# Optimization experiments

Measured on AMD Instinct MI355X. Metric: run time of the kernel, lower is better.

The kernel has to match this reference:

```python
import jax, jax.numpy as jnp
import numpy as np

THRESHOLD = 1.0  # LIF firing threshold (single-step LIF: spike = heaviside(v - thr))


def _lif_spike(v):
    # single-step LIF: membrane = input, spike where membrane exceeds threshold
    return (v > THRESHOLD).astype(v.dtype)


def setup_inputs() -> dict:
    key = jax.random.key(0)
    ks = jax.random.split(key, 9)
    B, T, C = 2, 2048, 1024
    s = 1.0 / np.sqrt(C)
    return {
        "x": jax.random.normal(ks[0], (B, T, C), dtype=jnp.float32),
        "Wq": jax.random.normal(ks[1], (C, C), dtype=jnp.float32) * s,
        "bq": jnp.zeros((C,), dtype=jnp.float32),
        "Wk": jax.random.normal(ks[2], (C, C), dtype=jnp.float32) * s,
        "bk": jnp.zeros((C,), dtype=jnp.float32),
        "Wv": jax.random.normal(ks[3], (C, C), dtype=jnp.float32) * s,
        "bv": jnp.zeros((C,), dtype=jnp.float32),
        "Wo": jax.random.normal(ks[4], (C, C), dtype=jnp.float32) * s,
        "bo": jnp.zeros((C,), dtype=jnp.float32),
    }


def reference(x, Wq, bq, Wk, bk, Wv, bv, Wo, bo):
    B, T, C = x.shape
    H = 16
    D = C // H
    q = x @ Wq.T + bq
    k = x @ Wk.T + bk
    v = x @ Wv.T + bv
    # LIF spiking on q and k (binary spikes)
    qs = _lif_spike(q).reshape(B, T, H, D).transpose(0, 2, 1, 3)  # [B,H,T,D]
    ks = _lif_spike(k).reshape(B, T, H, D).transpose(0, 2, 1, 3)  # [B,H,T,D]
    vh = v.reshape(B, T, H, D).transpose(0, 2, 1, 3)              # [B,H,T,D]
    scores = jnp.einsum('bhqd,bhkd->bhqk', qs, ks) / jnp.sqrt(jnp.asarray(D, x.dtype))
    attn = jax.nn.softmax(scores, axis=-1)
    out = jnp.einsum('bhqk,bhkd->bhqd', attn, vh)                 # [B,H,T,D]
    out = out.transpose(0, 2, 1, 3).reshape(B, T, C)
    return out @ Wo.T + bo
```

## Files before the change

kernel.cpp:

```cpp
#include <hip/hip_runtime.h>
#include <cstdint>

typedef unsigned long long u64;
typedef unsigned int u32;
typedef unsigned short u16;
typedef __attribute__((ext_vector_type(8))) u16 u16x8;
typedef __attribute__((ext_vector_type(4))) u16 u16x4;
typedef __attribute__((ext_vector_type(8))) _Float16 f16x8;
typedef __attribute__((ext_vector_type(4))) float f32x4;

#define T_LEN 2048
#define C_DIM 1024
#define H_NUM 16
#define M_ROWS 4096
#define MB (1024ull * 1024ull)
#define TAU 3e-3f
#define FCAP 65536u
#define BLK_FCAP 512u

__device__ __forceinline__ u16 f2bf(float f) {
  unsigned u = __builtin_bit_cast(unsigned, f);
  return (u16)((u + 0x7FFFu + ((u >> 16) & 1u)) >> 16);
}
__device__ __forceinline__ u16 f2h(float f) {
  _Float16 h = (_Float16)f;
  return __builtin_bit_cast(u16, h);
}

__device__ __forceinline__ void async16(u16* lds, const u16* g) {
  __builtin_amdgcn_global_load_lds(
      (const __attribute__((address_space(1))) void*)g,
      (__attribute__((address_space(3))) void*)lds, 16, 0, 0);
}

__global__ __launch_bounds__(256) void split_all(
    const float* __restrict__ x,  const float* __restrict__ Wq,
    const float* __restrict__ Wk, const float* __restrict__ Wv,
    const float* __restrict__ Wo,
    u16* xh, u16* wq16, u16* wk16, u16* wv16, u16* woh, u32* flagcnt)
{
  const int i = blockIdx.x * 256 + threadIdx.x;
  if (i == 0) *flagcnt = 0;
  const float* src; u16* dst; int off; int isbf = 0;
  if      (i < 1048576) { src = x;  dst = xh;   off = i; }
  else if (i < 1310720) { src = Wq; dst = wq16; off = i - 1048576; }
  else if (i < 1572864) { src = Wk; dst = wk16; off = i - 1310720; }
  else if (i < 1835008) { src = Wv; dst = wv16; off = i - 1572864; }
  else                  { src = Wo; dst = woh;  off = i - 1835008; isbf = 1; }
  const float4 v = ((const float4*)src)[off];
  u16x4 h;
  if (isbf) {
    h[0] = f2bf(v.x); h[1] = f2bf(v.y); h[2] = f2bf(v.z); h[3] = f2bf(v.w);
  } else {
    h[0] = f2h(v.x);  h[1] = f2h(v.y);  h[2] = f2h(v.z);  h[3] = f2h(v.w);
  }
  ((u16x4*)dst)[off] = h;
}

__global__ __launch_bounds__(256) void mfma_qkv(
    const u16* __restrict__ A16,
    const u16* __restrict__ Bq16, const u16* __restrict__ Bk16,
    const u16* __restrict__ Bv16,
    const float* __restrict__ bq, const float* __restrict__ bk,
    const float* __restrict__ bv,
    u32* __restrict__ pbits, u32* __restrict__ flagcnt,
    u32* __restrict__ flaglist, u16* __restrict__ vT)
{
  __shared__ u16 Ahs[2][128][32];
  __shared__ u16 Bhs[2][64][32];
  __shared__ u32 fls[2 + BLK_FCAP];

  const int tid  = threadIdx.x;
  const int lane = tid & 63;
  const int w    = tid >> 6;
  const int wr   = w & 1;
  const int wc   = w >> 1;
  const int bm   = blockIdx.x * 128;
  const int bng  = blockIdx.y * 64;
  const int sel  = bng >> 10;
  const int bnl  = bng & 1023;

  const u16* Bh = (sel == 0) ? Bq16 : (sel == 1) ? Bk16 : Bv16;
  const float* bias = (sel == 0) ? bq : (sel == 1) ? bk : bv;

  if (tid == 0) fls[0] = 0;

  f32x4 acc[4][2];
  #pragma unroll
  for (int mf = 0; mf < 4; ++mf)
    #pragma unroll
    for (int nf = 0; nf < 2; ++nf) acc[mf][nf] = (f32x4){0.f, 0.f, 0.f, 0.f};

  const int sr = lane >> 2;
  const int sc = lane & 3;

#define STG(DST, SRC, TB, R0, KT)                                          \
  async16(&DST[(R0)][0],                                                   \
          &SRC[(size_t)((TB) + (R0) + sr) * 1024 + (KT) +                  \
               ((sc ^ ((((R0) + sr) >> 1) & 3)) << 3)]);

#define STAGE(B_, KT)                        \
  {                                          \
    STG(Ahs[B_], A16, bm, w * 32, KT);       \
    STG(Ahs[B_], A16, bm, w * 32 + 16, KT);  \
    STG(Bhs[B_], Bh, bnl, w * 16, KT);       \
  }

  STAGE(0, 0);
  __syncthreads();

  const int fr = lane & 15;
  const int fg = lane >> 4;
  int cur = 0;

  for (int kt = 0; kt < 1024; kt += 32) {
    if (kt + 32 < 1024) STAGE(cur ^ 1, kt + 32);

    f16x8 a_h[4], b_h[2];
    #pragma unroll
    for (int mf = 0; mf < 4; ++mf) {
      const int row = wr * 64 + mf * 16 + fr;
      const int cs = (fg ^ ((row >> 1) & 3)) << 3;
      a_h[mf] = __builtin_bit_cast(f16x8, *(const u16x8*)&Ahs[cur][row][cs]);
    }
    #pragma unroll
    for (int nf = 0; nf < 2; ++nf) {
      const int col = wc * 32 + nf * 16 + fr;
      const int cs = (fg ^ ((col >> 1) & 3)) << 3;
      b_h[nf] = __builtin_bit_cast(f16x8, *(const u16x8*)&Bhs[cur][col][cs]);
    }
    #pragma unroll
    for (int mf = 0; mf < 4; ++mf)
      #pragma unroll
      for (int nf = 0; nf < 2; ++nf)
        acc[mf][nf] = __builtin_amdgcn_mfma_f32_16x16x32_f16(a_h[mf], b_h[nf], acc[mf][nf], 0, 0, 0);
    __syncthreads();
    cur ^= 1;
  }
#undef STAGE
#undef STG

  if (sel < 2) {
    const int c0 = bnl + wc * 32 + fr;
    const int c1 = c0 + 16;
    const float bb0 = bias[c0];
    const float bb1 = bias[c1];
    const int head = bnl >> 6;
    #pragma unroll
    for (int mf = 0; mf < 4; ++mf) {
      const int row0 = bm + wr * 64 + mf * 16;
      #pragma unroll
      for (int j = 0; j < 4; ++j) {
        const float v0 = acc[mf][0][j] + bb0;
        const float v1 = acc[mf][1][j] + bb1;
        const u64 b0 = __ballot(v0 > 1.0f);
        const u64 b1 = __ballot(v1 > 1.0f);
        const int m = row0 + fg * 4 + j;
        if (fr == 0) {
          const u32 mask = (u32)((b0 >> (fg * 16)) & 0xFFFFu)
                         | ((u32)((b1 >> (fg * 16)) & 0xFFFFu) << 16);
          pbits[(((size_t)sel * 4096 + m) * 16 + head) * 2 + wc] = mask;
        }
        if (__builtin_fabsf(v0 - 1.0f) < TAU) {
          const u32 s = atomicAdd(&fls[0], 1u);
          if (s < BLK_FCAP) fls[2 + s] = ((u32)sel << 22) | ((u32)m << 10) | (u32)c0;
        }
        if (__builtin_fabsf(v1 - 1.0f) < TAU) {
          const u32 s = atomicAdd(&fls[0], 1u);
          if (s < BLK_FCAP) fls[2 + s] = ((u32)sel << 22) | ((u32)m << 10) | (u32)c1;
        }
      }
    }
    __syncthreads();
    const u32 cnt = fls[0] < BLK_FCAP ? fls[0] : BLK_FCAP;
    if (tid == 0) fls[1] = atomicAdd(flagcnt, cnt);
    __syncthreads();
    const u32 base = fls[1];
    for (u32 i = tid; i < cnt; i += 256) {
      const u32 pos = base + i;
      if (pos < FCAP) flaglist[pos] = fls[2 + i];
    }
  } else {
    #pragma unroll
    for (int mf = 0; mf < 4; ++mf) {
      const int row0 = bm + wr * 64 + mf * 16 + fg * 4;
      #pragma unroll
      for (int nf = 0; nf < 2; ++nf) {
        const int col = bnl + wc * 32 + nf * 16 + fr;
        const float bb = bias[col];
        const int bb_ = row0 >> 11, t0 = row0 & 2047;
        const int hh = col >> 6, dd = col & 63;
        u16x4 o;
        o[0] = f2bf(acc[mf][nf][0] + bb);
        o[1] = f2bf(acc[mf][nf][1] + bb);
        o[2] = f2bf(acc[mf][nf][2] + bb);
        o[3] = f2bf(acc[mf][nf][3] + bb);
        *(u16x4*)&vT[(((size_t)(bb_ * 16 + hh)) * 64 + dd) * 2048 + t0] = o;
      }
    }
  }
}

__global__ __launch_bounds__(256) void fix_bits(
    const float* __restrict__ x,
    const float* __restrict__ Wq, const float* __restrict__ Wk,
    const float* __restrict__ bq, const float* __restrict__ bk,
    u32* __restrict__ pbits,
    const u32* __restrict__ flagcnt, const u32* __restrict__ flaglist)
{
  u32 cnt = *flagcnt;
  if (cnt > FCAP) cnt = FCAP;
  const int lane = threadIdx.x & 63;
  const u32 wid  = (blockIdx.x * 256 + threadIdx.x) >> 6;
  const u32 nw   = gridDim.x * 4;
  for (u32 i = wid; i < cnt; i += nw) {
    const u32 e = flaglist[i];
    const int which = e >> 22;
    const int m = (e >> 10) & 4095;
    const int n = e & 1023;
    const float* W    = which ? Wk : Wq;
    const float* bias = which ? bk : bq;
    float s = 0.f;
    #pragma unroll
    for (int j = 0; j < 16; ++j)
      s += x[(size_t)m * 1024 + lane + j * 64] * W[(size_t)n * 1024 + lane + j * 64];
    #pragma unroll
    for (int off = 32; off > 0; off >>= 1) s += __shfl_xor(s, off);
    const float val = s + bias[n];
    if (lane == 0) {
      const size_t idx = (((size_t)which * 4096 + m) * 16 + (n >> 6)) * 2 + ((n >> 5) & 1);
      const u32 bit = 1u << (n & 31);
      const bool oldb = (pbits[idx] >> (n & 31)) & 1u;
      const bool newb = val > 1.0f;
      if (oldb != newb) atomicXor(&pbits[idx], bit);
    }
  }
}

__global__ __launch_bounds__(256) void attn_mfma(
    const u32* __restrict__ pbits, const u16* __restrict__ vT,
    u16* __restrict__ oh)
{
  __shared__ u16 vtb[64][72];
  __shared__ u64 kbt[68];
  __shared__ u32 wt_tab[65];

  const int tid = threadIdx.x, lane = tid & 63, w = tid >> 6;
  const int bid = ((blockIdx.x & 7) << 7) | (blockIdx.x >> 3);
  const int qt = bid & 31, bh = bid >> 5, b = bh >> 4, h = bh & 15;

  const int fr = lane & 15, fg = lane >> 4;

  if (tid < 65)
    wt_tab[tid] = __builtin_bit_cast(u32, exp2f((float)tid * 0.1803368801f));

  const int qm = b * T_LEN + qt * 64 + w * 16 + fr;
  const size_t qbase = (((size_t)qm) * 16 + h) * 2;
  const u32 qlo = pbits[qbase];
  const u32 qhi = pbits[qbase + 1];

  f32x4 acc[4];
  #pragma unroll
  for (int nf = 0; nf < 4; ++nf) acc[nf] = (f32x4){0.f, 0.f, 0.f, 0.f};
  f32x4 acc_z = (f32x4){0.f, 0.f, 0.f, 0.f};

  u16x8 ones;
  #pragma unroll
  for (int j = 0; j < 8; ++j) ones[j] = 0x3F80;

  const u16* vbase = vT + (size_t)bh * 64 * T_LEN;
  const int sd = tid >> 2, sk = (tid & 3) << 3;

  for (int kt = 0; kt < T_LEN; kt += 64) {
    *(u16x8*)&vtb[sd][sk]      = *(const u16x8*)&vbase[(size_t)sd * T_LEN + kt + sk];
    *(u16x8*)&vtb[sd][sk + 32] = *(const u16x8*)&vbase[(size_t)sd * T_LEN + kt + sk + 32];
    if (tid < 64) {
      const int km = b * T_LEN + kt + tid;
      const size_t kb = (((size_t)(4096 + km)) * 16 + h) * 2;
      kbt[tid + (tid >> 4)] = (u64)pbits[kb] | ((u64)pbits[kb + 1] << 32);
    }
    __syncthreads();

    __builtin_amdgcn_s_setprio(1);
    #pragma unroll
    for (int ks = 0; ks < 2; ++ks) {
      u16x8 af;
      u32* afw = (u32*)&af;
      #pragma unroll
      for (int p = 0; p < 4; ++p) {
        const int kk = ks * 32 + fg * 8 + p * 2;
        const int pidx = kk + (kk >> 4);
        const u64 kb0 = kbt[pidx];
        const u64 kb1 = kbt[pidx + 1];
        const int mm0 = __builtin_popcount(qlo & (u32)kb0)
                      + __builtin_popcount(qhi & (u32)(kb0 >> 32));
        const int mm1 = __builtin_popcount(qlo & (u32)kb1)
                      + __builtin_popcount(qhi & (u32)(kb1 >> 32));
        const u32 t0 = wt_tab[mm0];
        const u32 t1 = wt_tab[mm1];
        afw[p] = (t1 & 0xFFFF0000u) | (t0 >> 16);
      }
      #pragma unroll
      for (int nf = 0; nf < 4; ++nf) {
        const u16x8 bfv = *(const u16x8*)&vtb[nf * 16 + fr][ks * 32 + fg * 8];
        acc[nf] = __builtin_amdgcn_mfma_f32_16x16x32_bf16(af, bfv, acc[nf], 0, 0, 0);
      }
      acc_z = __builtin_amdgcn_mfma_f32_16x16x32_bf16(af, ones, acc_z, 0, 0, 0);
    }
    __builtin_amdgcn_s_setprio(0);
    __syncthreads();
  }

  float invZ[4];
  #pragma unroll
  for (int j = 0; j < 4; ++j) invZ[j] = 1.0f / acc_z[j];

  #pragma unroll
  for (int nf = 0; nf < 4; ++nf) {
    const int col = h * 64 + nf * 16 + fr;
    #pragma unroll
    for (int j = 0; j < 4; ++j) {
      const int qrow = w * 16 + fg * 4 + j;
      const float o = acc[nf][j] * invZ[j];
      const size_t gq = (size_t)b * T_LEN + qt * 64 + qrow;
      oh[gq * 1024 + col] = f2bf(o);
    }
  }
}

__global__ __launch_bounds__(256) void mfma_out(
    const u16* __restrict__ Ah, const u16* __restrict__ Bh,
    const float* __restrict__ bias, float* __restrict__ out)
{
  __shared__ u16 Ahs[2][128][32];
  __shared__ u16 Bhs[2][64][32];

  const int tid  = threadIdx.x;
  const int lane = tid & 63;
  const int w    = tid >> 6;
  const int wr   = w & 1;
  const int wc   = w >> 1;
  const int bm   = blockIdx.x * 128;
  const int bn   = blockIdx.y * 64;

  f32x4 acc[4][2];
  #pragma unroll
  for (int mf = 0; mf < 4; ++mf)
    #pragma unroll
    for (int nf = 0; nf < 2; ++nf) acc[mf][nf] = (f32x4){0.f, 0.f, 0.f, 0.f};

  const int sr = lane >> 2;
  const int sc = lane & 3;

#define STG(DST, SRC, TB, R0, KT)                                          \
  async16(&DST[(R0)][0],                                                   \
          &SRC[(size_t)((TB) + (R0) + sr) * 1024 + (KT) +                  \
               ((sc ^ ((((R0) + sr) >> 1) & 3)) << 3)]);

#define STAGE(B_, KT)                        \
  {                                          \
    STG(Ahs[B_], Ah, bm, w * 32, KT);        \
    STG(Ahs[B_], Ah, bm, w * 32 + 16, KT);   \
    STG(Bhs[B_], Bh, bn, w * 16, KT);        \
  }

  STAGE(0, 0);
  __syncthreads();

  const int fr = lane & 15;
  const int fg = lane >> 4;
  int cur = 0;

  for (int kt = 0; kt < 1024; kt += 32) {
    if (kt + 32 < 1024) STAGE(cur ^ 1, kt + 32);

    u16x8 a_h[4], b_h[2];
    #pragma unroll
    for (int mf = 0; mf < 4; ++mf) {
      const int row = wr * 64 + mf * 16 + fr;
      const int cs = (fg ^ ((row >> 1) & 3)) << 3;
      a_h[mf] = *(const u16x8*)&Ahs[cur][row][cs];
    }
    #pragma unroll
    for (int nf = 0; nf < 2; ++nf) {
      const int col = wc * 32 + nf * 16 + fr;
      const int cs = (fg ^ ((col >> 1) & 3)) << 3;
      b_h[nf] = *(const u16x8*)&Bhs[cur][col][cs];
    }
    #pragma unroll
    for (int mf = 0; mf < 4; ++mf)
      #pragma unroll
      for (int nf = 0; nf < 2; ++nf)
        acc[mf][nf] = __builtin_amdgcn_mfma_f32_16x16x32_bf16(a_h[mf], b_h[nf], acc[mf][nf], 0, 0, 0);
    __syncthreads();
    cur ^= 1;
  }
#undef STAGE
#undef STG

  #pragma unroll
  for (int mf = 0; mf < 4; ++mf) {
    const int row0 = bm + wr * 64 + mf * 16 + fg * 4;
    #pragma unroll
    for (int nf = 0; nf < 2; ++nf) {
      const int col = bn + wc * 32 + nf * 16 + fr;
      const float bb = bias[col];
      #pragma unroll
      for (int j = 0; j < 4; ++j)
        out[(size_t)(row0 + j) * 1024 + col] = acc[mf][nf][j] + bb;
    }
  }
}

extern "C" void kernel_launch(void* const* d_in, const int* in_sizes, int n_in,
                              void* d_out, int out_size, void* d_ws, size_t ws_size,
                              hipStream_t stream) {
  const float* x  = (const float*)d_in[0];
  const float* Wq = (const float*)d_in[1];
  const float* bq = (const float*)d_in[2];
  const float* Wk = (const float*)d_in[3];
  const float* bk = (const float*)d_in[4];
  const float* Wv = (const float*)d_in[5];
  const float* bv = (const float*)d_in[6];
  const float* Wo = (const float*)d_in[7];
  const float* bo = (const float*)d_in[8];
  float* out = (float*)d_out;

  char* ws = (char*)d_ws;
  u16* oh   = (u16*)ws;
  u16* xh   = (u16*)(ws + 16 * MB);
  u16* vT   = (u16*)(ws + 32 * MB);
  u16* Woh  = (u16*)(ws + 40 * MB);
  u32* pbits = (u32*)(ws + 44 * MB);
  u32* flagcnt  = (u32*)(ws + 45 * MB);
  u32* flaglist = (u32*)(ws + 45 * MB + 256);

  char* dob = (char*)d_out;
  u16* Wq16 = (u16*)dob;
  u16* Wk16 = (u16*)(dob + 2 * MB);
  u16* Wv16 = (u16*)(dob + 4 * MB);

  split_all<<<8192, 256, 0, stream>>>(x, Wq, Wk, Wv, Wo,
                                      xh, Wq16, Wk16, Wv16, Woh, flagcnt);

  dim3 g1(M_ROWS / 128, 3072 / 64);
  mfma_qkv<<<g1, 256, 0, stream>>>(xh, Wq16, Wk16, Wv16,
                                   bq, bk, bv, pbits, flagcnt, flaglist, vT);

  fix_bits<<<256, 256, 0, stream>>>(x, Wq, Wk, bq, bk, pbits, flagcnt, flaglist);

  attn_mfma<<<32 * 32, 256, 0, stream>>>(pbits, vT, oh);

  dim3 g2(M_ROWS / 128, 1024 / 64);
  mfma_out<<<g2, 256, 0, stream>>>(oh, Woh, bo, out);
}
```

Measured before the change: 164.9 us.

## Widen QKV GEMM tile and pipeline attention loads with larger key tiles

The QKV projection kernel now computes 128x128 output tiles per block instead of 128x64, halving the grid and raising the MFMA count per A-tile load. The attention kernel processes 128 keys per iteration, prefetches the next V and key-bit tile into registers before the barrier, reads key bits as vectorized 16-byte LDS loads, and computes exp2 inline instead of through a shared lookup table. These changes target global-load latency and per-iteration sync overhead, at the cost of more registers (possible occupancy loss) and fewer QKV blocks.

```diff
diff --git a/kernel.cpp b/kernel.cpp
--- a/kernel.cpp
+++ b/kernel.cpp
@@ -6,6 +6,7 @@
 typedef unsigned short u16;
 typedef __attribute__((ext_vector_type(8))) u16 u16x8;
 typedef __attribute__((ext_vector_type(4))) u16 u16x4;
+typedef __attribute__((ext_vector_type(2))) u64 u64x2;
 typedef __attribute__((ext_vector_type(8))) _Float16 f16x8;
 typedef __attribute__((ext_vector_type(4))) float f32x4;
 
@@ -67,7 +68,7 @@
     u32* __restrict__ flaglist, u16* __restrict__ vT)
 {
   __shared__ u16 Ahs[2][128][32];
-  __shared__ u16 Bhs[2][64][32];
+  __shared__ u16 Bhs[2][128][32];
   __shared__ u32 fls[2 + BLK_FCAP];
 
   const int tid  = threadIdx.x;
@@ -76,7 +77,7 @@
   const int wr   = w & 1;
   const int wc   = w >> 1;
   const int bm   = blockIdx.x * 128;
-  const int bng  = blockIdx.y * 64;
+  const int bng  = blockIdx.y * 128;
   const int sel  = bng >> 10;
   const int bnl  = bng & 1023;
 
@@ -85,11 +86,11 @@
 
   if (tid == 0) fls[0] = 0;
 
-  f32x4 acc[4][2];
+  f32x4 acc[4][4];
   #pragma unroll
   for (int mf = 0; mf < 4; ++mf)
     #pragma unroll
-    for (int nf = 0; nf < 2; ++nf) acc[mf][nf] = (f32x4){0.f, 0.f, 0.f, 0.f};
+    for (int nf = 0; nf < 4; ++nf) acc[mf][nf] = (f32x4){0.f, 0.f, 0.f, 0.f};
 
   const int sr = lane >> 2;
   const int sc = lane & 3;
@@ -99,11 +100,12 @@
           &SRC[(size_t)((TB) + (R0) + sr) * 1024 + (KT) +                  \
                ((sc ^ ((((R0) + sr) >> 1) & 3)) << 3)]);
 
-#define STAGE(B_, KT)                        \
-  {                                          \
-    STG(Ahs[B_], A16, bm, w * 32, KT);       \
-    STG(Ahs[B_], A16, bm, w * 32 + 16, KT);  \
-    STG(Bhs[B_], Bh, bnl, w * 16, KT);       \
+#define STAGE(B_, KT)                          \
+  {                                            \
+    STG(Ahs[B_], A16, bm, w * 32, KT);         \
+    STG(Ahs[B_], A16, bm, w * 32 + 16, KT);    \
+    STG(Bhs[B_], Bh, bnl, w * 32, KT);         \
+    STG(Bhs[B_], Bh, bnl, w * 32 + 16, KT);    \
   }
 
   STAGE(0, 0);
@@ -116,7 +118,7 @@
   for (int kt = 0; kt < 1024; kt += 32) {
     if (kt + 32 < 1024) STAGE(cur ^ 1, kt + 32);
 
-    f16x8 a_h[4], b_h[2];
+    f16x8 a_h[4], b_h[4];
     #pragma unroll
     for (int mf = 0; mf < 4; ++mf) {
       const int row = wr * 64 + mf * 16 + fr;
@@ -124,15 +126,15 @@
       a_h[mf] = __builtin_bit_cast(f16x8, *(const u16x8*)&Ahs[cur][row][cs]);
     }
     #pragma unroll
-    for (int nf = 0; nf < 2; ++nf) {
-      const int col = wc * 32 + nf * 16 + fr;
+    for (int nf = 0; nf < 4; ++nf) {
+      const int col = wc * 64 + nf * 16 + fr;
       const int cs = (fg ^ ((col >> 1) & 3)) << 3;
       b_h[nf] = __builtin_bit_cast(f16x8, *(const u16x8*)&Bhs[cur][col][cs]);
     }
     #pragma unroll
     for (int mf = 0; mf < 4; ++mf)
       #pragma unroll
-      for (int nf = 0; nf < 2; ++nf)
+      for (int nf = 0; nf < 4; ++nf)
         acc[mf][nf] = __builtin_amdgcn_mfma_f32_16x16x32_f16(a_h[mf], b_h[nf], acc[mf][nf], 0, 0, 0);
     __syncthreads();
     cur ^= 1;
@@ -141,33 +143,38 @@
 #undef STG
 
   if (sel < 2) {
-    const int c0 = bnl + wc * 32 + fr;
-    const int c1 = c0 + 16;
-    const float bb0 = bias[c0];
-    const float bb1 = bias[c1];
-    const int head = bnl >> 6;
+    float bb[4];
+    #pragma unroll
+    for (int nf = 0; nf < 4; ++nf) bb[nf] = bias[bnl + wc * 64 + nf * 16 + fr];
     #pragma unroll
     for (int mf = 0; mf < 4; ++mf) {
       const int row0 = bm + wr * 64 + mf * 16;
       #pragma unroll
       for (int j = 0; j < 4; ++j) {
-        const float v0 = acc[mf][0][j] + bb0;
-        const float v1 = acc[mf][1][j] + bb1;
-        const u64 b0 = __ballot(v0 > 1.0f);
-        const u64 b1 = __ballot(v1 > 1.0f);
         const int m = row0 + fg * 4 + j;
+        float v[4];
+        u64 bl[4];
+        #pragma unroll
+        for (int nf = 0; nf < 4; ++nf) {
+          v[nf] = acc[mf][nf][j] + bb[nf];
+          bl[nf] = __ballot(v[nf] > 1.0f);
+        }
         if (fr == 0) {
-          const u32 mask = (u32)((b0 >> (fg * 16)) & 0xFFFFu)
-                         | ((u32)((b1 >> (fg * 16)) & 0xFFFFu) << 16);
-          pbits[(((size_t)sel * 4096 + m) * 16 + head) * 2 + wc] = mask;
+          #pragma unroll
+          for (int nfp = 0; nfp < 2; ++nfp) {
+            const u32 mask = (u32)((bl[2 * nfp] >> (fg * 16)) & 0xFFFFu)
+                           | ((u32)((bl[2 * nfp + 1] >> (fg * 16)) & 0xFFFFu) << 16);
+            const int cb = bnl + wc * 64 + nfp * 32;
+            pbits[(((size_t)sel * 4096 + m) * 16 + (cb >> 6)) * 2 + ((cb >> 5) & 1)] = mask;
+          }
         }
-        if (__builtin_fabsf(v0 - 1.0f) < TAU) {
-          const u32 s = atomicAdd(&fls[0], 1u);
-          if (s < BLK_FCAP) fls[2 + s] = ((u32)sel << 22) | ((u32)m << 10) | (u32)c0;
-        }
-        if (__builtin_fabsf(v1 - 1.0f) < TAU) {
-          const u32 s = atomicAdd(&fls[0], 1u);
-          if (s < BLK_FCAP) fls[2 + s] = ((u32)sel << 22) | ((u32)m << 10) | (u32)c1;
+        #pragma unroll
+        for (int nf = 0; nf < 4; ++nf) {
+          if (__builtin_fabsf(v[nf] - 1.0f) < TAU) {
+            const u32 s = atomicAdd(&fls[0], 1u);
+            const u32 cc = (u32)(bnl + wc * 64 + nf * 16 + fr);
+            if (s < BLK_FCAP) fls[2 + s] = ((u32)sel << 22) | ((u32)m << 10) | cc;
+          }
         }
       }
     }
@@ -185,16 +192,16 @@
     for (int mf = 0; mf < 4; ++mf) {
       const int row0 = bm + wr * 64 + mf * 16 + fg * 4;
       #pragma unroll
-      for (int nf = 0; nf < 2; ++nf) {
-        const int col = bnl + wc * 32 + nf * 16 + fr;
-        const float bb = bias[col];
+      for (int nf = 0; nf < 4; ++nf) {
+        const int col = bnl + wc * 64 + nf * 16 + fr;
+        const float bbv = bias[col];
         const int bb_ = row0 >> 11, t0 = row0 & 2047;
         const int hh = col >> 6, dd = col & 63;
         u16x4 o;
-        o[0] = f2bf(acc[mf][nf][0] + bb);
-        o[1] = f2bf(acc[mf][nf][1] + bb);
-        o[2] = f2bf(acc[mf][nf][2] + bb);
-        o[3] = f2bf(acc[mf][nf][3] + bb);
+        o[0] = f2bf(acc[mf][nf][0] + bbv);
+        o[1] = f2bf(acc[mf][nf][1] + bbv);
+        o[2] = f2bf(acc[mf][nf][2] + bbv);
+        o[3] = f2bf(acc[mf][nf][3] + bbv);
         *(u16x4*)&vT[(((size_t)(bb_ * 16 + hh)) * 64 + dd) * 2048 + t0] = o;
       }
     }
@@ -241,18 +248,14 @@
     const u32* __restrict__ pbits, const u16* __restrict__ vT,
     u16* __restrict__ oh)
 {
-  __shared__ u16 vtb[64][72];
-  __shared__ u64 kbt[68];
-  __shared__ u32 wt_tab[65];
+  __shared__ u16 vtb[64][136];
+  __shared__ u64 kbt[128];
 
   const int tid = threadIdx.x, lane = tid & 63, w = tid >> 6;
   const int bid = ((blockIdx.x & 7) << 7) | (blockIdx.x >> 3);
   const int qt = bid & 31, bh = bid >> 5, b = bh >> 4, h = bh & 15;
 
   const int fr = lane & 15, fg = lane >> 4;
-
-  if (tid < 65)
-    wt_tab[tid] = __builtin_bit_cast(u32, exp2f((float)tid * 0.1803368801f));
 
   const int qm = b * T_LEN + qt * 64 + w * 16 + fr;
   const size_t qbase = (((size_t)qm) * 16 + h) * 2;
@@ -271,33 +274,53 @@
   const u16* vbase = vT + (size_t)bh * 64 * T_LEN;
   const int sd = tid >> 2, sk = (tid & 3) << 3;
 
-  for (int kt = 0; kt < T_LEN; kt += 64) {
-    *(u16x8*)&vtb[sd][sk]      = *(const u16x8*)&vbase[(size_t)sd * T_LEN + kt + sk];
-    *(u16x8*)&vtb[sd][sk + 32] = *(const u16x8*)&vbase[(size_t)sd * T_LEN + kt + sk + 32];
-    if (tid < 64) {
-      const int km = b * T_LEN + kt + tid;
-      const size_t kb = (((size_t)(4096 + km)) * 16 + h) * 2;
-      kbt[tid + (tid >> 4)] = (u64)pbits[kb] | ((u64)pbits[kb + 1] << 32);
-    }
+  u16x8 r0, r1, r2, r3;
+  u64 kbr = 0;
+#define VLOAD(KT)                                                       \
+  {                                                                     \
+    r0 = *(const u16x8*)&vbase[(size_t)sd * T_LEN + (KT) + sk];         \
+    r1 = *(const u16x8*)&vbase[(size_t)sd * T_LEN + (KT) + sk + 32];    \
+    r2 = *(const u16x8*)&vbase[(size_t)sd * T_LEN + (KT) + sk + 64];    \
+    r3 = *(const u16x8*)&vbase[(size_t)sd * T_LEN + (KT) + sk + 96];    \
+  }
+#define KLOAD(KT)                                                       \
+  if (tid < 128) {                                                      \
+    const int km = b * T_LEN + (KT) + tid;                              \
+    const size_t kb = (((size_t)(4096 + km)) * 16 + h) * 2;             \
+    kbr = (u64)pbits[kb] | ((u64)pbits[kb + 1] << 32);                  \
+  }
+
+  VLOAD(0);
+  KLOAD(0);
+
+  for (int kt = 0; kt < T_LEN; kt += 128) {
+    *(u16x8*)&vtb[sd][sk]      = r0;
+    *(u16x8*)&vtb[sd][sk + 32] = r1;
+    *(u16x8*)&vtb[sd][sk + 64] = r2;
+    *(u16x8*)&vtb[sd][sk + 96] = r3;
+    if (tid < 128) kbt[tid] = kbr;
+    if (kt + 128 < T_LEN) { VLOAD(kt + 128); KLOAD(kt + 128); }
     __syncthreads();
 
     __builtin_amdgcn_s_setprio(1);
     #pragma unroll
-    for (int ks = 0; ks < 2; ++ks) {
+    for (int ks = 0; ks < 4; ++ks) {
+      u64 kreg[8];
+      const int kb0 = ks * 32 + fg * 8;
+      *(u64x2*)&kreg[0] = *(const u64x2*)&kbt[kb0];
+      *(u64x2*)&kreg[2] = *(const u64x2*)&kbt[kb0 + 2];
+      *(u64x2*)&kreg[4] = *(const u64x2*)&kbt[kb0 + 4];
+      *(u64x2*)&kreg[6] = *(const u64x2*)&kbt[kb0 + 6];
       u16x8 af;
       u32* afw = (u32*)&af;
       #pragma unroll
       for (int p = 0; p < 4; ++p) {
-        const int kk = ks * 32 + fg * 8 + p * 2;
-        const int pidx = kk + (kk >> 4);
-        const u64 kb0 = kbt[pidx];
-        const u64 kb1 = kbt[pidx + 1];
-        const int mm0 = __builtin_popcount(qlo & (u32)kb0)
-                      + __builtin_popcount(qhi & (u32)(kb0 >> 32));
-        const int mm1 = __builtin_popcount(qlo & (u32)kb1)
-                      + __builtin_popcount(qhi & (u32)(kb1 >> 32));
-        const u32 t0 = wt_tab[mm0];
-        const u32 t1 = wt_tab[mm1];
+        const int mm0 = __builtin_popcount(qlo & (u32)kreg[2 * p])
+                      + __builtin_popcount(qhi & (u32)(kreg[2 * p] >> 32));
+        const int mm1 = __builtin_popcount(qlo & (u32)kreg[2 * p + 1])
+                      + __builtin_popcount(qhi & (u32)(kreg[2 * p + 1] >> 32));
+        const u32 t0 = __builtin_bit_cast(u32, exp2f((float)mm0 * 0.1803368801f));
+        const u32 t1 = __builtin_bit_cast(u32, exp2f((float)mm1 * 0.1803368801f));
         afw[p] = (t1 & 0xFFFF0000u) | (t0 >> 16);
       }
       #pragma unroll
@@ -310,6 +333,8 @@
     __builtin_amdgcn_s_setprio(0);
     __syncthreads();
   }
+#undef VLOAD
+#undef KLOAD
 
   float invZ[4];
   #pragma unroll
@@ -443,7 +468,7 @@
   split_all<<<8192, 256, 0, stream>>>(x, Wq, Wk, Wv, Wo,
                                       xh, Wq16, Wk16, Wv16, Woh, flagcnt);
 
-  dim3 g1(M_ROWS / 128, 3072 / 64);
+  dim3 g1(M_ROWS / 128, 3072 / 128);
   mfma_qkv<<<g1, 256, 0, stream>>>(xh, Wq16, Wk16, Wv16,
                                    bq, bk, bv, pbits, flagcnt, flaglist, vT);
 
```

Result: slower. 173.4 us (+5.1%).
